# Optimization experiments

Hardware: AMD Instinct MI355X
Metric: run time of the kernel (lower is better)

Reference implementation:

```python
import jax, jax.numpy as jnp
import numpy as np

T, V, D = 16, 1024, 128  # number_steps, number_vectors, latent_dimension
B = 2048
EPS = 1e-12  # tf.nn.l2_normalize epsilon


def _l2_normalize(x, axis=-1):
    sq = jnp.sum(jnp.square(x), axis=axis, keepdims=True)
    return x * jax.lax.rsqrt(jnp.maximum(sq, EPS))


def setup_inputs() -> dict:
    key = jax.random.key(0)
    k1, k2, k3 = jax.random.split(key, 3)
    inputs = jax.random.normal(k1, (B, D, 1), dtype=jnp.float32)
    index = jax.random.randint(k2, (B,), 0, T, dtype=jnp.int64)
    # glorot_uniform over (T, V, D): limit = sqrt(6 / (fan_in + fan_out))
    limit = float(np.sqrt(6.0 / (V + D)))
    latent_vectors = jax.random.uniform(k3, (T, V, D), minval=-limit, maxval=limit, dtype=jnp.float32)
    return {"inputs": inputs, "latent_vectors": latent_vectors, "index": index}


def reference(inputs, latent_vectors, index):
    x = jnp.squeeze(inputs, axis=-1)                 # (B, D)
    cur = latent_vectors[index]                      # (B, V, D) gather over steps
    xn = _l2_normalize(x, axis=-1)                   # (B, D)
    ln = _l2_normalize(cur, axis=-1)                 # (B, V, D)
    sim = jnp.einsum('bvd,bd->bv', ln, xn)           # cosine similarity (B, V)
    best = jnp.argmax(sim, axis=-1)                  # (B,)
    sel = jnp.take_along_axis(cur, best[:, None, None], axis=1)  # (B, 1, D)
    return jnp.squeeze(sel, axis=1)                  # (B, D)
```

## Files before the change

kernel.cpp:

```cpp
#include <hip/hip_runtime.h>
#include <cstdint>

#define T_STEPS 16
#define V_VECS  1024
#define D_DIM   128
#define B_BATCH 2048
#define BCAP    2048

__global__ __launch_bounds__(256) void k_score(const float* __restrict__ X,
                                               const float* __restrict__ L,
                                               const int* __restrict__ idx,
                                               unsigned long long* __restrict__ partial,
                                               int* __restrict__ counts) {
    __shared__ __align__(16) float As[D_DIM][64];
    __shared__ __align__(16) float Xs[D_DIM][64];
    __shared__ float npart[4][64];
    __shared__ float invn_s[64];
    __shared__ unsigned short blist[BCAP];
    __shared__ int wcnt[8][4];

    const int t    = blockIdx.y;
    const int vt   = blockIdx.x;
    const int v0   = vt * 64;
    const int z    = blockIdx.z;
    const int tid  = threadIdx.x;
    const int lane = tid & 63;
    const int w    = tid >> 6;

    bool mm[8]; int wpre[8];
    #pragma unroll
    for (int r = 0; r < 8; ++r) {
        const bool m = (idx[r * 256 + tid] == t);
        const unsigned long long bal = __ballot(m);
        mm[r]   = m;
        wpre[r] = __popcll(bal & ((1ull << lane) - 1ull));
        if (lane == 0) wcnt[r][w] = __popcll(bal);
    }
    __syncthreads();
    int run = 0;
    #pragma unroll
    for (int r = 0; r < 8; ++r) {
        int base = run;
        #pragma unroll
        for (int w2 = 0; w2 < 4; ++w2) {
            const int c = wcnt[r][w2];
            if (w2 < w) base += c;
            run += c;
        }
        if (mm[r]) blist[base + wpre[r]] = (unsigned short)(r * 256 + tid);
    }
    const int n = run;
    if (vt == 0 && z == 0 && tid == 0) counts[t] = n;
    if (z * 64 >= n) return;

    const float4* LA = (const float4*)(L + (size_t)(t * V_VECS + v0) * D_DIM);
    float ss = 0.f;
    #pragma unroll
    for (int p = 0; p < 8; ++p) {
        const int k4 = w + 4 * p;
        const float4 g = LA[lane * 32 + k4];
        As[4 * k4 + 0][lane] = g.x;
        As[4 * k4 + 1][lane] = g.y;
        As[4 * k4 + 2][lane] = g.z;
        As[4 * k4 + 3][lane] = g.w;
        ss += g.x * g.x + g.y * g.y + g.z * g.z + g.w * g.w;
    }
    npart[w][lane] = ss;
    __syncthreads();
    if (tid < 64) {
        const float s = npart[0][tid] + npart[1][tid] + npart[2][tid] + npart[3][tid];
        invn_s[tid] = rsqrtf(fmaxf(s, 1e-12f));
    }

    const int tv = tid & 15;
    const int tb = tid >> 4;
    const float4* XA = (const float4*)X;

    for (int cs = z * 64; cs < n; cs += 128) {
        __syncthreads();

        const int brow = cs + lane;
        const int bg = (brow < n) ? (int)blist[brow] : -1;
        const float4* xr = XA + (size_t)(bg < 0 ? 0 : bg) * 32;
        #pragma unroll
        for (int p = 0; p < 8; ++p) {
            const int k4 = w + 4 * p;
            float4 g = make_float4(0.f, 0.f, 0.f, 0.f);
            if (bg >= 0) g = xr[k4];
            Xs[4 * k4 + 0][lane] = g.x;
            Xs[4 * k4 + 1][lane] = g.y;
            Xs[4 * k4 + 2][lane] = g.z;
            Xs[4 * k4 + 3][lane] = g.w;
        }
        __syncthreads();

        float acc[4][4] = {};
        #pragma unroll 16
        for (int k = 0; k < D_DIM; ++k) {
            const float4 av = *(const float4*)&As[k][tv * 4];
            const float4 xb = *(const float4*)&Xs[k][tb * 4];
            const float a[4] = {av.x, av.y, av.z, av.w};
            const float x[4] = {xb.x, xb.y, xb.z, xb.w};
            #pragma unroll
            for (int i = 0; i < 4; ++i)
                #pragma unroll
                for (int j = 0; j < 4; ++j)
                    acc[i][j] += a[i] * x[j];
        }

        const float4 inv4 = *(const float4*)&invn_s[tv * 4];
        const float invp[4] = {inv4.x, inv4.y, inv4.z, inv4.w};

        #pragma unroll
        for (int j = 0; j < 4; ++j) {
            float s = acc[0][j] * invp[0];
            int   c = v0 + tv * 4;
            #pragma unroll
            for (int i = 1; i < 4; ++i) {
                const float si = acc[i][j] * invp[i];
                const int   ci = v0 + tv * 4 + i;
                if (si > s) { s = si; c = ci; }
            }
            #pragma unroll
            for (int m = 8; m >= 1; m >>= 1) {
                const float u  = __shfl_xor(s, m);
                const int   cu = __shfl_xor(c, m);
                if (u > s || (u == s && cu < c)) { s = u; c = cu; }
            }
            if (tv == 0) {
                const int bi = cs + tb * 4 + j;
                if (bi < n) {
                    unsigned int ub = __float_as_uint(s);
                    ub = (ub & 0x80000000u) ? ~ub : (ub | 0x80000000u);
                    const unsigned long long key =
                        ((unsigned long long)ub << 32) |
                        ((unsigned long long)(unsigned)(1023 - c) << 16) |
                        (unsigned long long)blist[bi];
                    partial[((size_t)vt * T_STEPS + t) * BCAP + bi] = key;
                }
            }
        }
    }
}

__global__ __launch_bounds__(256) void k_gather(const float* __restrict__ L,
                                                const int* __restrict__ counts,
                                                const unsigned long long* __restrict__ partial,
                                                float* __restrict__ out) {
    __shared__ int vArr[64];
    __shared__ int bArr[64];

    const int t  = blockIdx.y;
    const int cs = blockIdx.x * 64;
    const int n  = counts[t];
    if (cs >= n) return;

    const int tid = threadIdx.x;
    const int nb  = min(64, n - cs);
    if (tid < nb) {
        const int bi = cs + tid;
        unsigned long long best = partial[(size_t)t * BCAP + bi];
        #pragma unroll
        for (int q = 1; q < 16; ++q) {
            const unsigned long long k2 =
                partial[((size_t)q * T_STEPS + t) * BCAP + bi];
            if (k2 > best) best = k2;
        }
        vArr[tid] = 1023 - (int)((best >> 16) & 0xffffull);
        bArr[tid] = (int)(best & 0xffffull);
    }
    __syncthreads();

    const int l32 = tid & 31;
    for (int q = tid >> 5; q < nb; q += 8) {
        const int b = bArr[q], v = vArr[q];
        ((float4*)out)[b * 32 + l32] =
            ((const float4*)L)[(size_t)(t * V_VECS + v) * 32 + l32];
    }
}

extern "C" void kernel_launch(void* const* d_in, const int* in_sizes, int n_in,
                              void* d_out, int out_size, void* d_ws, size_t ws_size,
                              hipStream_t stream) {
    const float* X  = (const float*)d_in[0];
    const float* L  = (const float*)d_in[1];
    const int* idx  = (const int*)d_in[2];
    float* out      = (float*)d_out;

    char* ws = (char*)d_ws;
    int* counts               = (int*)ws;
    unsigned long long* part  = (unsigned long long*)(ws + 4096);

    hipLaunchKernelGGL(k_score,  dim3(16, 16, 2), dim3(256), 0, stream,
                       X, L, idx, part, counts);
    hipLaunchKernelGGL(k_gather, dim3(32, 16),    dim3(256), 0, stream,
                       L, counts, part, out);
}
```

Measured before the change: 28.02 us.

## Rebalance score chunks across z-blocks, prefetch latent tile, shrink gather grid

Latent tile loads are issued into registers before the index ballot/compaction, so their global latency overlaps that work. The batch-chunk schedule is changed: each z block does one 64-row chunk, both then split the rows 128..191 into a 32-row half-chunk with a 4x2 micro-tile, and continue from 192 in 128-row strides. This balances the ~128-row per-step workload across the two z blocks instead of leaving one idle. The gather kernel uses a 3-wide grid with a strided loop instead of 32 mostly-empty blocks, at the cost of extra register pressure and more code paths.

```diff
diff --git a/kernel.cpp b/kernel.cpp
--- a/kernel.cpp
+++ b/kernel.cpp
@@ -27,6 +27,11 @@
     const int lane = tid & 63;
     const int w    = tid >> 6;
 
+    const float4* LA = (const float4*)(L + (size_t)(t * V_VECS + v0) * D_DIM);
+    float4 areg[8];
+    #pragma unroll
+    for (int p = 0; p < 8; ++p) areg[p] = LA[lane * 32 + (w + 4 * p)];
+
     bool mm[8]; int wpre[8];
     #pragma unroll
     for (int r = 0; r < 8; ++r) {
@@ -53,12 +58,11 @@
     if (vt == 0 && z == 0 && tid == 0) counts[t] = n;
     if (z * 64 >= n) return;
 
-    const float4* LA = (const float4*)(L + (size_t)(t * V_VECS + v0) * D_DIM);
     float ss = 0.f;
     #pragma unroll
     for (int p = 0; p < 8; ++p) {
         const int k4 = w + 4 * p;
-        const float4 g = LA[lane * 32 + k4];
+        const float4 g = areg[p];
         As[4 * k4 + 0][lane] = g.x;
         As[4 * k4 + 1][lane] = g.y;
         As[4 * k4 + 2][lane] = g.z;
@@ -76,7 +80,9 @@
     const int tb = tid >> 4;
     const float4* XA = (const float4*)X;
 
-    for (int cs = z * 64; cs < n; cs += 128) {
+    int cs = z * 64;
+    bool first = true;
+    while (cs < n) {
         __syncthreads();
 
         const int brow = cs + lane;
@@ -140,6 +146,78 @@
                 }
             }
         }
+        cs = first ? (192 + z * 64) : (cs + 128);
+        first = false;
+    }
+
+    const int hs = 128 + z * 32;
+    if (hs < n) {
+        __syncthreads();
+
+        const int hrow = tid >> 3;
+        const int hk8  = tid & 7;
+        const int hb   = hs + hrow;
+        const int hbg  = (hb < n) ? (int)blist[hb] : -1;
+        const float4* hxr = XA + (size_t)(hbg < 0 ? 0 : hbg) * 32;
+        #pragma unroll
+        for (int p = 0; p < 4; ++p) {
+            const int k4 = hk8 + 8 * p;
+            float4 g = make_float4(0.f, 0.f, 0.f, 0.f);
+            if (hbg >= 0) g = hxr[k4];
+            Xs[4 * k4 + 0][hrow] = g.x;
+            Xs[4 * k4 + 1][hrow] = g.y;
+            Xs[4 * k4 + 2][hrow] = g.z;
+            Xs[4 * k4 + 3][hrow] = g.w;
+        }
+        __syncthreads();
+
+        const int tb2 = tid >> 4;
+        float hacc[4][2] = {};
+        #pragma unroll 16
+        for (int k = 0; k < D_DIM; ++k) {
+            const float4 av = *(const float4*)&As[k][tv * 4];
+            const float2 xb = *(const float2*)&Xs[k][tb2 * 2];
+            const float a[4] = {av.x, av.y, av.z, av.w};
+            const float x[2] = {xb.x, xb.y};
+            #pragma unroll
+            for (int i = 0; i < 4; ++i)
+                #pragma unroll
+                for (int j = 0; j < 2; ++j)
+                    hacc[i][j] += a[i] * x[j];
+        }
+
+        const float4 inv4 = *(const float4*)&invn_s[tv * 4];
+        const float invp[4] = {inv4.x, inv4.y, inv4.z, inv4.w};
+
+        #pragma unroll
+        for (int j = 0; j < 2; ++j) {
+            float s = hacc[0][j] * invp[0];
+            int   c = v0 + tv * 4;
+            #pragma unroll
+            for (int i = 1; i < 4; ++i) {
+                const float si = hacc[i][j] * invp[i];
+                const int   ci = v0 + tv * 4 + i;
+                if (si > s) { s = si; c = ci; }
+            }
+            #pragma unroll
+            for (int m = 8; m >= 1; m >>= 1) {
+                const float u  = __shfl_xor(s, m);
+                const int   cu = __shfl_xor(c, m);
+                if (u > s || (u == s && cu < c)) { s = u; c = cu; }
+            }
+            if (tv == 0) {
+                const int bi = hs + tb2 * 2 + j;
+                if (bi < n) {
+                    unsigned int ub = __float_as_uint(s);
+                    ub = (ub & 0x80000000u) ? ~ub : (ub | 0x80000000u);
+                    const unsigned long long key =
+                        ((unsigned long long)ub << 32) |
+                        ((unsigned long long)(unsigned)(1023 - c) << 16) |
+                        (unsigned long long)blist[bi];
+                    partial[((size_t)vt * T_STEPS + t) * BCAP + bi] = key;
+                }
+            }
+        }
     }
 }
 
@@ -150,32 +228,32 @@
     __shared__ int vArr[64];
     __shared__ int bArr[64];
 
-    const int t  = blockIdx.y;
-    const int cs = blockIdx.x * 64;
-    const int n  = counts[t];
-    if (cs >= n) return;
-
+    const int t   = blockIdx.y;
+    const int n   = counts[t];
     const int tid = threadIdx.x;
-    const int nb  = min(64, n - cs);
-    if (tid < nb) {
-        const int bi = cs + tid;
-        unsigned long long best = partial[(size_t)t * BCAP + bi];
-        #pragma unroll
-        for (int q = 1; q < 16; ++q) {
-            const unsigned long long k2 =
-                partial[((size_t)q * T_STEPS + t) * BCAP + bi];
-            if (k2 > best) best = k2;
-        }
-        vArr[tid] = 1023 - (int)((best >> 16) & 0xffffull);
-        bArr[tid] = (int)(best & 0xffffull);
-    }
-    __syncthreads();
-
     const int l32 = tid & 31;
-    for (int q = tid >> 5; q < nb; q += 8) {
-        const int b = bArr[q], v = vArr[q];
-        ((float4*)out)[b * 32 + l32] =
-            ((const float4*)L)[(size_t)(t * V_VECS + v) * 32 + l32];
+
+    for (int cs = blockIdx.x * 64; cs < n; cs += 192) {
+        const int nb = min(64, n - cs);
+        if (tid < nb) {
+            const int bi = cs + tid;
+            unsigned long long best = partial[(size_t)t * BCAP + bi];
+            #pragma unroll
+            for (int q = 1; q < 16; ++q) {
+                const unsigned long long k2 =
+                    partial[((size_t)q * T_STEPS + t) * BCAP + bi];
+                if (k2 > best) best = k2;
+            }
+            vArr[tid] = 1023 - (int)((best >> 16) & 0xffffull);
+            bArr[tid] = (int)(best & 0xffffull);
+        }
+        __syncthreads();
+        for (int q = tid >> 5; q < nb; q += 8) {
+            const int b = bArr[q], v = vArr[q];
+            ((float4*)out)[b * 32 + l32] =
+                ((const float4*)L)[(size_t)(t * V_VECS + v) * 32 + l32];
+        }
+        __syncthreads();
     }
 }
 
@@ -193,6 +271,6 @@
 
     hipLaunchKernelGGL(k_score,  dim3(16, 16, 2), dim3(256), 0, stream,
                        X, L, idx, part, counts);
-    hipLaunchKernelGGL(k_gather, dim3(32, 16),    dim3(256), 0, stream,
+    hipLaunchKernelGGL(k_gather, dim3(3, 16),     dim3(256), 0, stream,
                        L, counts, part, out);
 }
```

New measurement: 25.63 us. -8.5%, faster.

## Shrink shared memory, prefetch L tile early, raise z-split and shrink gather grid

Applied to the files above, without the earlier changes.

The scoring kernel now stages the batch tile in two halves of 64 rows, sharing one buffer with the norm partials and warp counts to cut LDS use, and requests 3 blocks per CU via launch bounds. The latent tile load is issued before the index scan so its latency overlaps the ballot work, and indices are read as int4 vectors, which changes the batch order in blist. The z split grows from 2 to 3 and the gather kernel uses a grid-stride loop over 3 blocks per step instead of 32. Together these trade extra barriers and register pressure for higher occupancy, and the smaller gather grid may serialize its work.

```diff
diff --git a/kernel.cpp b/kernel.cpp
--- a/kernel.cpp
+++ b/kernel.cpp
@@ -7,17 +7,19 @@
 #define B_BATCH 2048
 #define BCAP    2048
 
-__global__ __launch_bounds__(256) void k_score(const float* __restrict__ X,
-                                               const float* __restrict__ L,
-                                               const int* __restrict__ idx,
-                                               unsigned long long* __restrict__ partial,
-                                               int* __restrict__ counts) {
+__global__ __launch_bounds__(256, 3) void k_score(const float* __restrict__ X,
+                                                  const float* __restrict__ L,
+                                                  const int* __restrict__ idx,
+                                                  unsigned long long* __restrict__ partial,
+                                                  int* __restrict__ counts) {
     __shared__ __align__(16) float As[D_DIM][64];
-    __shared__ __align__(16) float Xs[D_DIM][64];
-    __shared__ float npart[4][64];
+    __shared__ __align__(16) char  xs_mem[64 * 64 * 4];
     __shared__ float invn_s[64];
     __shared__ unsigned short blist[BCAP];
-    __shared__ int wcnt[8][4];
+
+    float (*Xs)[64]    = (float(*)[64])xs_mem;
+    float (*npart)[64] = (float(*)[64])xs_mem;
+    int   (*wcnt)[4]   = (int(*)[4])(xs_mem + 1024);
 
     const int t    = blockIdx.y;
     const int vt   = blockIdx.x;
@@ -27,10 +29,19 @@
     const int lane = tid & 63;
     const int w    = tid >> 6;
 
+    const float4* LA = (const float4*)(L + (size_t)(t * V_VECS + v0) * D_DIM);
+    float4 areg[8];
+    #pragma unroll
+    for (int p = 0; p < 8; ++p) areg[p] = LA[lane * 32 + (w + 4 * p)];
+
+    const int4* idx4 = (const int4*)idx;
+    const int4 ia = idx4[tid * 2];
+    const int4 ib = idx4[tid * 2 + 1];
+    const int iv8[8] = {ia.x, ia.y, ia.z, ia.w, ib.x, ib.y, ib.z, ib.w};
     bool mm[8]; int wpre[8];
     #pragma unroll
     for (int r = 0; r < 8; ++r) {
-        const bool m = (idx[r * 256 + tid] == t);
+        const bool m = (iv8[r] == t);
         const unsigned long long bal = __ballot(m);
         mm[r]   = m;
         wpre[r] = __popcll(bal & ((1ull << lane) - 1ull));
@@ -47,18 +58,17 @@
             if (w2 < w) base += c;
             run += c;
         }
-        if (mm[r]) blist[base + wpre[r]] = (unsigned short)(r * 256 + tid);
+        if (mm[r]) blist[base + wpre[r]] = (unsigned short)(tid * 8 + r);
     }
     const int n = run;
     if (vt == 0 && z == 0 && tid == 0) counts[t] = n;
     if (z * 64 >= n) return;
 
-    const float4* LA = (const float4*)(L + (size_t)(t * V_VECS + v0) * D_DIM);
     float ss = 0.f;
     #pragma unroll
     for (int p = 0; p < 8; ++p) {
         const int k4 = w + 4 * p;
-        const float4 g = LA[lane * 32 + k4];
+        const float4 g = areg[p];
         As[4 * k4 + 0][lane] = g.x;
         As[4 * k4 + 1][lane] = g.y;
         As[4 * k4 + 2][lane] = g.z;
@@ -76,36 +86,42 @@
     const int tb = tid >> 4;
     const float4* XA = (const float4*)X;
 
-    for (int cs = z * 64; cs < n; cs += 128) {
-        __syncthreads();
-
+    for (int cs = z * 64; cs < n; cs += 192) {
         const int brow = cs + lane;
         const int bg = (brow < n) ? (int)blist[brow] : -1;
         const float4* xr = XA + (size_t)(bg < 0 ? 0 : bg) * 32;
+
+        float acc[4][4] = {};
+
         #pragma unroll
-        for (int p = 0; p < 8; ++p) {
-            const int k4 = w + 4 * p;
-            float4 g = make_float4(0.f, 0.f, 0.f, 0.f);
-            if (bg >= 0) g = xr[k4];
-            Xs[4 * k4 + 0][lane] = g.x;
-            Xs[4 * k4 + 1][lane] = g.y;
-            Xs[4 * k4 + 2][lane] = g.z;
-            Xs[4 * k4 + 3][lane] = g.w;
-        }
-        __syncthreads();
-
-        float acc[4][4] = {};
-        #pragma unroll 16
-        for (int k = 0; k < D_DIM; ++k) {
-            const float4 av = *(const float4*)&As[k][tv * 4];
-            const float4 xb = *(const float4*)&Xs[k][tb * 4];
-            const float a[4] = {av.x, av.y, av.z, av.w};
-            const float x[4] = {xb.x, xb.y, xb.z, xb.w};
-            #pragma unroll
-            for (int i = 0; i < 4; ++i)
+        for (int h = 0; h < 2; ++h) {
+            __syncthreads();
+
+            #pragma unroll
+            for (int p = 0; p < 4; ++p) {
+                const int k4l = w + 4 * p;
+                float4 g = make_float4(0.f, 0.f, 0.f, 0.f);
+                if (bg >= 0) g = xr[h * 16 + k4l];
+                Xs[4 * k4l + 0][lane] = g.x;
+                Xs[4 * k4l + 1][lane] = g.y;
+                Xs[4 * k4l + 2][lane] = g.z;
+                Xs[4 * k4l + 3][lane] = g.w;
+            }
+            __syncthreads();
+
+            #pragma unroll 16
+            for (int kl = 0; kl < 64; ++kl) {
+                const int kg = h * 64 + kl;
+                const float4 av = *(const float4*)&As[kg][tv * 4];
+                const float4 xb = *(const float4*)&Xs[kl][tb * 4];
+                const float a[4] = {av.x, av.y, av.z, av.w};
+                const float x[4] = {xb.x, xb.y, xb.z, xb.w};
                 #pragma unroll
-                for (int j = 0; j < 4; ++j)
-                    acc[i][j] += a[i] * x[j];
+                for (int i = 0; i < 4; ++i)
+                    #pragma unroll
+                    for (int j = 0; j < 4; ++j)
+                        acc[i][j] += a[i] * x[j];
+            }
         }
 
         const float4 inv4 = *(const float4*)&invn_s[tv * 4];
@@ -150,32 +166,32 @@
     __shared__ int vArr[64];
     __shared__ int bArr[64];
 
-    const int t  = blockIdx.y;
-    const int cs = blockIdx.x * 64;
-    const int n  = counts[t];
-    if (cs >= n) return;
-
+    const int t   = blockIdx.y;
+    const int n   = counts[t];
     const int tid = threadIdx.x;
-    const int nb  = min(64, n - cs);
-    if (tid < nb) {
-        const int bi = cs + tid;
-        unsigned long long best = partial[(size_t)t * BCAP + bi];
-        #pragma unroll
-        for (int q = 1; q < 16; ++q) {
-            const unsigned long long k2 =
-                partial[((size_t)q * T_STEPS + t) * BCAP + bi];
-            if (k2 > best) best = k2;
-        }
-        vArr[tid] = 1023 - (int)((best >> 16) & 0xffffull);
-        bArr[tid] = (int)(best & 0xffffull);
-    }
-    __syncthreads();
-
     const int l32 = tid & 31;
-    for (int q = tid >> 5; q < nb; q += 8) {
-        const int b = bArr[q], v = vArr[q];
-        ((float4*)out)[b * 32 + l32] =
-            ((const float4*)L)[(size_t)(t * V_VECS + v) * 32 + l32];
+
+    for (int cs = blockIdx.x * 64; cs < n; cs += 192) {
+        const int nb = min(64, n - cs);
+        if (tid < nb) {
+            const int bi = cs + tid;
+            unsigned long long best = partial[(size_t)t * BCAP + bi];
+            #pragma unroll
+            for (int q = 1; q < 16; ++q) {
+                const unsigned long long k2 =
+                    partial[((size_t)q * T_STEPS + t) * BCAP + bi];
+                if (k2 > best) best = k2;
+            }
+            vArr[tid] = 1023 - (int)((best >> 16) & 0xffffull);
+            bArr[tid] = (int)(best & 0xffffull);
+        }
+        __syncthreads();
+        for (int q = tid >> 5; q < nb; q += 8) {
+            const int b = bArr[q], v = vArr[q];
+            ((float4*)out)[b * 32 + l32] =
+                ((const float4*)L)[(size_t)(t * V_VECS + v) * 32 + l32];
+        }
+        __syncthreads();
     }
 }
 
@@ -191,8 +207,8 @@
     int* counts               = (int*)ws;
     unsigned long long* part  = (unsigned long long*)(ws + 4096);
 
-    hipLaunchKernelGGL(k_score,  dim3(16, 16, 2), dim3(256), 0, stream,
+    hipLaunchKernelGGL(k_score,  dim3(16, 16, 3), dim3(256), 0, stream,
                        X, L, idx, part, counts);
-    hipLaunchKernelGGL(k_gather, dim3(32, 16),    dim3(256), 0, stream,
+    hipLaunchKernelGGL(k_gather, dim3(3, 16),     dim3(256), 0, stream,
                        L, counts, part, out);
 }
```

Result: faster. 26.94 us (-3.8%).
